# Optimization experiments

Measured on AMD Instinct MI355X. Metric: run time of the kernel, lower is better.

## Reference

```python
import jax, jax.numpy as jnp
import numpy as np
from jax import lax

B, H, W, C = 8, 128, 128, 256
HEADS, WIN, PRETRAIN = 8, 8, 8
QK_U = C // HEADS            # 32
QK_CH = QK_U * HEADS         # 256
KV_CH = QK_CH + C            # 512
BLOCK = WIN // 2             # key block size at half resolution
HALO = WIN                   # halo window (halo_window//2) at half resolution
PAD = (HALO - BLOCK) // 2    # halo overlap pad at half resolution


def _win_part(x, heads):
    b, h, w, c = x.shape
    u = c // heads
    x = x.reshape(b, h // WIN, WIN, w // WIN, WIN, heads, u)
    x = x.transpose(0, 1, 3, 5, 2, 4, 6)
    return x.reshape(b, (h // WIN) * (w // WIN), heads, WIN * WIN, u)


def _halo_part(x):
    # overlapping halo blocks: [b,hh,wh,c] -> [b, nw, HALO*HALO, c]
    b, h, w, c = x.shape
    xp = jnp.pad(x, ((0, 0), (PAD, PAD), (PAD, PAD), (0, 0)))
    hb, wb = h // BLOCK, w // BLOCK
    ih = jnp.arange(hb)[:, None] * BLOCK + jnp.arange(HALO)[None, :]
    iw = jnp.arange(wb)[:, None] * BLOCK + jnp.arange(HALO)[None, :]
    t = xp[:, ih][:, :, :, iw]            # [b, hb, HALO, wb, HALO, c]
    t = t.transpose(0, 1, 3, 2, 4, 5)
    return t.reshape(b, hb * wb, HALO * HALO, c)


def _halo_part_fused(x, heads):
    t = _halo_part(x)
    b, nw, l, c = t.shape
    u = c // heads
    return t.reshape(b, nw, l, heads, u).transpose(0, 1, 3, 2, 4)


def _l2n(x):
    # tf.math.l2_normalize with epsilon=1.55e-5
    return x * lax.rsqrt(jnp.maximum(jnp.sum(x * x, -1, keepdims=True), 1.55e-5))


def _rel_bias(cpb_w1, cpb_b1, cpb_w2):
    # Swin-V2 style continuous (log-CPB) relative bias between full-res query
    # window and half-res halo key window.
    qc = jnp.arange(WIN, dtype=jnp.float32)
    kc = (jnp.arange(HALO, dtype=jnp.float32) - PAD) * 2.0 + 0.5  # half-res centers in full-res coords
    r1 = qc[:, None] - kc[None, :]
    rel_y = jnp.broadcast_to(r1[:, None, :, None], (WIN, WIN, HALO, HALO))
    rel_x = jnp.broadcast_to(r1[None, :, None, :], (WIN, WIN, HALO, HALO))
    rel = jnp.stack([rel_y, rel_x], -1).reshape(WIN * WIN, HALO * HALO, 2)
    rel = rel / (PRETRAIN - 1) * 8.0
    rel = jnp.sign(rel) * jnp.log2(jnp.abs(rel) + 1.0) / np.float32(np.log2(8.0))
    hmid = jax.nn.relu(rel @ cpb_w1 + cpb_b1)
    bias = 16.0 * jax.nn.sigmoid(hmid @ cpb_w2)   # [q, k, heads]
    return bias.transpose(2, 0, 1)[None, None]    # [1,1,heads,q,k]


def _pad_mask(dtype):
    # No outer divisible-pad here (H,W divisible), but halo zero-padding at the
    # image border must be masked out (-100 on out-of-image key positions).
    m = jnp.ones((1, H // 2, W // 2, 1), dtype)   # min-pooled validity map (all ones)
    hm = _halo_part(m)                            # [1, nw, HALO*HALO, 1]; border halos -> 0
    return -100.0 * (hm[..., 0] == 0).astype(dtype)[:, :, None, None, :]  # [1,nw,1,1,k]


def reference(inputs, qkv_w, q_bias, v_bias, dw_w, dw_gamma, dw_beta, dw_mean, dw_var, scale, cpb_w1, cpb_b1, cpb_w2, proj_w, proj_b):
    qkv = jnp.einsum('bhwc,cd->bhwd', inputs, qkv_w)
    q, kv = qkv[..., :QK_CH], qkv[..., QK_CH:]
    # depthwise 3x3 stride-2 conv + (inference) batch-norm on K/V path
    kv = lax.conv_general_dilated(kv, dw_w, (2, 2), 'SAME',
                                  dimension_numbers=('NHWC', 'HWIO', 'NHWC'),
                                  feature_group_count=KV_CH)
    kv = (kv - dw_mean) * lax.rsqrt(dw_var + 1e-3) * dw_gamma + dw_beta
    q = q + q_bias
    kv = kv + jnp.concatenate([jnp.zeros_like(q_bias), v_bias])
    qw = _win_part(q, HEADS)                                 # [B,nw,h,64,QK_U]
    k = _halo_part_fused(kv[..., :QK_CH], HEADS)             # [B,nw,h,64,QK_U]
    v = _halo_part_fused(kv[..., QK_CH:], HEADS)             # [B,nw,h,64,V_U]
    logit_scale = jnp.exp(jnp.minimum(scale, np.float32(np.log(100.0))))  # [h,1,1]
    attn = jnp.einsum('bnhqd,bnhkd->bnhqk', _l2n(qw) * logit_scale, _l2n(k))
    attn = attn + _rel_bias(cpb_w1, cpb_b1, cpb_w2) + _pad_mask(attn.dtype)
    attn = jax.nn.softmax(attn, axis=-1)
    out = jnp.einsum('bnhqk,bnhkd->bnhqd', attn, v)
    hb, wb = H // WIN, W // WIN
    out = out.reshape(B, hb, wb, HEADS, WIN, WIN, C // HEADS)
    out = out.transpose(0, 1, 4, 2, 5, 3, 6).reshape(B, H, W, C)
    return jnp.einsum('bhwc,cd->bhwd', out, proj_w) + proj_b


def setup_inputs() -> dict:
    key = jax.random.key(0)
    ks = jax.random.split(key, 16)
    rn = lambda k, s, sc=0.05: jax.random.normal(k, s, jnp.float32) * sc
    return {
        'inputs': jax.random.normal(ks[0], (B, H, W, C), jnp.float32),
        'qkv_w': rn(ks[1], (C, 2 * QK_CH + C)),
        'q_bias': rn(ks[2], (QK_CH,)),
        'v_bias': rn(ks[3], (C,)),
        'dw_w': rn(ks[4], (3, 3, 1, KV_CH)),
        'dw_gamma': 1.0 + rn(ks[5], (KV_CH,)),
        'dw_beta': rn(ks[6], (KV_CH,)),
        'dw_mean': rn(ks[7], (KV_CH,)),
        'dw_var': jax.random.uniform(ks[8], (KV_CH,), jnp.float32, 0.5, 1.5),
        'scale': jnp.full((HEADS, 1, 1), np.log(10.0), jnp.float32),
        'cpb_w1': rn(ks[9], (2, 512), 0.5),
        'cpb_b1': rn(ks[10], (512,), 0.1),
        'cpb_w2': rn(ks[11], (512, HEADS), 0.1),
        'proj_w': rn(ks[12], (C, C)),
        'proj_b': rn(ks[13], (C,)),
    }
```

## Files before the change

kernel.cpp:

```cpp
#include <hip/hip_runtime.h>
#include <stdint.h>


typedef __attribute__((ext_vector_type(8))) short short8;
typedef __attribute__((ext_vector_type(4))) short short4v;
typedef __attribute__((ext_vector_type(4))) float f32x4;

#define VT_PLANE 4624L

__device__ __forceinline__ float bf2f(unsigned short u){
  union { unsigned int i; float f; } x; x.i = ((unsigned int)u)<<16; return x.f;
}
__device__ __forceinline__ unsigned short f2bf(float f){
  union { float f; unsigned int i; } x; x.f = f;
  unsigned int r = x.i + 0x7FFFu + ((x.i>>16)&1u);
  return (unsigned short)(r>>16);
}
__device__ __forceinline__ unsigned int pack_bf_t(float a, float b){
  union { float f; unsigned int u; } x, y; x.f = a; y.f = b;
  return (y.u & 0xFFFF0000u) | (x.u >> 16);
}
__device__ __forceinline__ void gl_lds16(const void* g, void* l){
  __builtin_amdgcn_global_load_lds((const __attribute__((address_space(1))) unsigned int*)g,
                                   (__attribute__((address_space(3))) unsigned int*)l, 16, 0, 0);
}

__global__ __launch_bounds__(256) void cvt_bf16_kernel(const float* __restrict__ in,
                                                       short* __restrict__ out, long n8)
{
  long stride = (long)gridDim.x * 256;
  for (long i = (long)blockIdx.x*256 + threadIdx.x; i < n8; i += stride){
    float4 a = ((const float4*)in)[2*i];
    float4 b = ((const float4*)in)[2*i+1];
    short8 v;
    v[0]=(short)f2bf(a.x); v[1]=(short)f2bf(a.y); v[2]=(short)f2bf(a.z); v[3]=(short)f2bf(a.w);
    v[4]=(short)f2bf(b.x); v[5]=(short)f2bf(b.y); v[6]=(short)f2bf(b.z); v[7]=(short)f2bf(b.w);
    ((short8*)out)[i] = v;
  }
}

__global__ void transpose_w_kernel(const float* __restrict__ w, short* __restrict__ wt,
                                   int K, int N)
{
  int idx = blockIdx.x*256 + threadIdx.x;
  if (idx >= K*N) return;
  int n = idx / K, k = idx - n*K;
  wt[idx] = (short)f2bf(w[(long)k*N + n]);
}

__global__ __launch_bounds__(64) void relbias_kernel(const float* __restrict__ w1,
    const float* __restrict__ b1, const float* __restrict__ w2, float* __restrict__ out)
{
  int q = blockIdx.x;
  int k = threadIdx.x;
  float ry = (float)(q>>3) - (((float)(k>>3) - 2.f)*2.f + 0.5f);
  float rx = (float)(q&7)  - (((float)(k&7)  - 2.f)*2.f + 0.5f);
  ry *= (8.f/7.f); rx *= (8.f/7.f);
  float sy = (ry>0.f)?1.f:((ry<0.f)?-1.f:0.f);
  float sx = (rx>0.f)?1.f:((rx<0.f)?-1.f:0.f);
  ry = sy * log2f(fabsf(ry)+1.f) * (1.f/3.f);
  rx = sx * log2f(fabsf(rx)+1.f) * (1.f/3.f);
  float acc[8] = {0,0,0,0,0,0,0,0};
  for (int j=0;j<512;j++){
    float hm = ry*w1[j] + rx*w1[512+j] + b1[j];
    hm = fmaxf(hm, 0.f);
#pragma unroll
    for (int h=0;h<8;h++) acc[h] += hm * w2[j*8+h];
  }
#pragma unroll
  for (int h=0;h<8;h++)
    out[h*4096 + q*64 + k] = (16.f / (1.f + __expf(-acc[h]))) * 1.4426950408889634f;
}

template<int ND, int OUTMODE>
__global__ __launch_bounds__(256) void gemm_bt_kernel(const short* __restrict__ A,
    const short* __restrict__ Bt, const float* __restrict__ bias,
    short* __restrict__ out_q, short* __restrict__ out_kv, float* __restrict__ out_f)
{
  __shared__ short smem[32768];
  const int tid  = threadIdx.x;
  const int lane = tid & 63;
  const int wid  = tid >> 6;
  const int wr = wid >> 1, wc = wid & 1;

  constexpr int NCB = ND / 128;
  const int bid = blockIdx.x;
  const int xcd = bid & 7;
  const int idx = bid >> 3;
  const long row0 = (long)(xcd * 128 + idx / NCB) * 128;
  const int  col0 = (idx % NCB) * 128;

  f32x4 acc[4][4];
#pragma unroll
  for (int m=0;m<4;m++)
#pragma unroll
    for (int n=0;n<4;n++) acc[m][n] = (f32x4){0.f,0.f,0.f,0.f};

  auto stage = [&](int buf, int kt){
#pragma unroll
    for (int j = 0; j < 4; j++) {
      int f = j*256 + tid;
      int r = f >> 3, p = f & 7;
      gl_lds16(A + (row0 + r)*256 + kt + ((p ^ (r&7))<<3),
               smem + buf*8192 + ((j*256 + (wid<<6))<<3));
      gl_lds16(Bt + (long)(col0 + r)*256 + kt + ((p ^ (r&7))<<3),
               smem + 16384 + buf*8192 + ((j*256 + (wid<<6))<<3));
    }
  };
  auto compute = [&](int buf){
    const short* As = smem + buf*8192;
    const short* Bs = smem + 16384 + buf*8192;
#pragma unroll
    for (int ks = 0; ks < 2; ks++) {
      short8 af[4], bfv[4];
#pragma unroll
      for (int m=0;m<4;m++){
        int r = wr*64 + m*16 + (lane & 15);
        int g = ks*4 + (lane >> 4);
        af[m] = *(const short8*)(As + r*64 + ((g ^ (r&7))<<3));
      }
#pragma unroll
      for (int n=0;n<4;n++){
        int r = wc*64 + n*16 + (lane & 15);
        int g = ks*4 + (lane >> 4);
        bfv[n] = *(const short8*)(Bs + r*64 + ((g ^ (r&7))<<3));
      }
#pragma unroll
      for (int m=0;m<4;m++)
#pragma unroll
        for (int n=0;n<4;n++)
          acc[m][n] = __builtin_amdgcn_mfma_f32_16x16x32_bf16(af[m], bfv[n], acc[m][n], 0, 0, 0);
    }
  };

  stage(0, 0);
  __syncthreads();
#pragma unroll
  for (int t = 0; t < 4; t++){
    if (t < 3) stage((t+1)&1, (t+1)*64);
    compute(t&1);
    __syncthreads();
  }

  if (OUTMODE == 0) {
    float bcol[4];
#pragma unroll
    for (int n=0;n<4;n++){
      int col = col0 + wc*64 + n*16 + (lane&15);
      bcol[n] = (col < 256) ? bias[col] : 0.f;
    }
#pragma unroll
    for (int m=0;m<4;m++){
#pragma unroll
      for (int n=0;n<4;n++){
        int col = wc*64 + n*16 + (lane&15);
        int cg = col >> 3;
#pragma unroll
        for (int rg=0;rg<4;rg++){
          int row = wr*64 + m*16 + ((lane>>4)<<2) + rg;
          smem[row*128 + ((cg ^ (row&7))<<3) + (col&7)] = (short)f2bf(acc[m][n][rg] + bcol[n]);
        }
      }
    }
    __syncthreads();
    int row = tid >> 1, ch = tid & 1;
    long grow = row0 + row;
#pragma unroll
    for (int j=0;j<8;j++){
      int cg = ch*8 + j;
      short8 v = *(const short8*)(smem + row*128 + ((cg ^ (row&7))<<3));
      int col = col0 + cg*8;
      if (col0 < 256) *(short8*)(out_q + grow*256 + col)        = v;
      else            *(short8*)(out_kv + grow*512 + (col-256)) = v;
    }
  } else {
    float* fs = (float*)smem;
#pragma unroll
    for (int m=0;m<4;m++){
#pragma unroll
      for (int n=0;n<4;n++){
        int col = wc*64 + n*16 + (lane&15);
        int c4 = col >> 2;
        float bv = bias[col0 + col];
#pragma unroll
        for (int rg=0;rg<4;rg++){
          int row = wr*64 + m*16 + ((lane>>4)<<2) + rg;
          fs[row*128 + ((c4 ^ (row&7))<<2) + (col&3)] = acc[m][n][rg] + bv;
        }
      }
    }
    __syncthreads();
    int row = tid >> 1;
    long grow = row0 + row;
#pragma unroll
    for (int j=0;j<16;j++){
      int c4 = (tid&1)*16 + j;
      float4 v = *(const float4*)(fs + row*128 + ((c4 ^ (row&7))<<2));
      *(float4*)(out_f + grow*ND + col0 + c4*4) = v;
    }
  }
}

__global__ __launch_bounds__(256) void dwconv_kernel(const short* __restrict__ kv_buf,
    const float* __restrict__ dw_w, const float* __restrict__ gamma,
    const float* __restrict__ beta, const float* __restrict__ mean,
    const float* __restrict__ var, const float* __restrict__ v_bias,
    short* __restrict__ kv_K, short* __restrict__ v_t)
{
  const int bid = blockIdx.x;
  const int b  = bid >> 7;
  const int rem = bid & 127;
  const int y2 = rem >> 1, xq = rem & 1;
  const int tid = threadIdx.x;
  const int lane = tid & 63, w = tid >> 6;
  const int ch0 = lane * 8;

  float s[8], sh[8];
#pragma unroll
  for (int i=0;i<8;i+=4){
    float4 g4 = *(const float4*)(gamma + ch0 + i);
    float4 v4 = *(const float4*)(var   + ch0 + i);
    float4 m4 = *(const float4*)(mean  + ch0 + i);
    float4 b4 = *(const float4*)(beta  + ch0 + i);
    float gg[4] = {g4.x,g4.y,g4.z,g4.w}, vv[4] = {v4.x,v4.y,v4.z,v4.w};
    float mm[4] = {m4.x,m4.y,m4.z,m4.w}, bb[4] = {b4.x,b4.y,b4.z,b4.w};
#pragma unroll
    for (int j=0;j<4;j++){
      float sv = gg[j] * rsqrtf(vv[j] + 1e-3f);
      s[i+j]  = sv;
      sh[i+j] = bb[j] - mm[j]*sv;
    }
  }
  if (ch0 >= 256){
    float4 vb0 = *(const float4*)(v_bias + ch0 - 256);
    float4 vb1 = *(const float4*)(v_bias + ch0 - 252);
    sh[0]+=vb0.x; sh[1]+=vb0.y; sh[2]+=vb0.z; sh[3]+=vb0.w;
    sh[4]+=vb1.x; sh[5]+=vb1.y; sh[6]+=vb1.z; sh[7]+=vb1.w;
  }

  float wv[9][8];
#pragma unroll
  for (int t=0;t<9;t++){
    float4 w0 = *(const float4*)(dw_w + t*512 + ch0);
    float4 w1 = *(const float4*)(dw_w + t*512 + ch0 + 4);
    wv[t][0]=w0.x; wv[t][1]=w0.y; wv[t][2]=w0.z; wv[t][3]=w0.w;
    wv[t][4]=w1.x; wv[t][5]=w1.y; wv[t][6]=w1.z; wv[t][7]=w1.w;
  }

  const int y0 = y2*2;
  const bool vy2 = (y0 + 2) < 128;
  const short* r0 = kv_buf + (((long)b*128 + y0)*128)*512 + ch0;
  const short* r1 = r0 + 128*512;
  const short* r2 = r1 + 128*512;
  const short8 zero8 = {0,0,0,0,0,0,0,0};

  const int x2base = xq*32 + w*8;
  const int xs = x2base*2;

  auto ld = [&](const short* r, int x, bool vy)->short8 {
    if (vy && x < 128) return *(const short8*)(r + (long)x*512);
    return zero8;
  };

  short8 L0 = ld(r0, xs, true), L1 = ld(r1, xs, true), L2 = ld(r2, xs, vy2);

  const int vc = ch0 - 256, hh = vc >> 5, d0 = vc & 31;
  const long vtb = ((long)((b*8+hh)*32 + d0))*VT_PLANE + (long)(y2+2)*68;

#pragma unroll
  for (int i=0;i<8;i++){
    const int x2 = x2base + i;
    const int xm = xs + 2*i + 1, xr = xs + 2*i + 2;
    short8 M0 = ld(r0, xm, true), M1 = ld(r1, xm, true), M2 = ld(r2, xm, vy2);
    short8 R0 = ld(r0, xr, true), R1 = ld(r1, xr, true), R2 = ld(r2, xr, vy2);

    float acc[8];
#pragma unroll
    for (int c=0;c<8;c++) acc[c] = 0.f;
#pragma unroll
    for (int c=0;c<8;c++){
      acc[c] += bf2f((unsigned short)L0[c]) * wv[0][c];
      acc[c] += bf2f((unsigned short)M0[c]) * wv[1][c];
      acc[c] += bf2f((unsigned short)R0[c]) * wv[2][c];
      acc[c] += bf2f((unsigned short)L1[c]) * wv[3][c];
      acc[c] += bf2f((unsigned short)M1[c]) * wv[4][c];
      acc[c] += bf2f((unsigned short)R1[c]) * wv[5][c];
      acc[c] += bf2f((unsigned short)L2[c]) * wv[6][c];
      acc[c] += bf2f((unsigned short)M2[c]) * wv[7][c];
      acc[c] += bf2f((unsigned short)R2[c]) * wv[8][c];
    }
    short8 o;
#pragma unroll
    for (int c=0;c<8;c++) o[c] = (short)f2bf(acc[c]*s[c] + sh[c]);

    if (ch0 < 256) {
      *(short8*)(kv_K + ((long)((b*64+y2)*64 + x2))*256 + ch0) = o;
    } else {
      long base = vtb + (x2+2);
#pragma unroll
      for (int c=0;c<8;c++) v_t[base + (long)c*VT_PLANE] = o[c];
    }
    L0 = R0; L1 = R1; L2 = R2;
  }
}

__global__ __launch_bounds__(256) void halo_attn_kernel(const short* __restrict__ q_buf,
    const short* __restrict__ kv_K, const short* __restrict__ v_t,
    const float* __restrict__ relb, const float* __restrict__ scale,
    short* __restrict__ attn_out)
{
  __shared__ short ps[4][4096];

  const int bid = blockIdx.x;
  const int b = bid >> 8, wno = bid & 255;
  const int bi = wno >> 4, bj = wno & 15;
  const int tid = threadIdx.x;
  const int w = tid >> 6, lane = tid & 63;
  const int g = lane >> 4, q15 = lane & 15;
  short* myps = &ps[w][0];
  const short8 zero8 = {0,0,0,0,0,0,0,0};

  long kbase[4]; bool kval[4];
#pragma unroll
  for (int m=0;m<4;m++){
    int key = m*16 + q15;
    int yy = bi*4-2 + (key>>3), xx = bj*4-2 + (key&7);
    kval[m] = (yy>=0 && yy<64 && xx>=0 && xx<64);
    kbase[m] = ((long)((b*64+yy)*64+xx))*256 + g*8;
  }
  float mkv[4][4];
#pragma unroll
  for (int m=0;m<4;m++)
#pragma unroll
    for (int r=0;r<4;r++){
      int key = m*16 + g*4 + r;
      int yy = bi*4-2+(key>>3), xx = bj*4-2+(key&7);
      mkv[m][r] = (yy>=0&&yy<64&&xx>=0&&xx<64) ? 0.f : -30000.f;
    }
  long qpix[4];
#pragma unroll
  for (int n=0;n<4;n++){
    int q = n*16+q15;
    qpix[n] = ((long)((b*128+bi*8+(q>>3))*128 + bj*8+(q&7)))*256;
  }
  int voff[2];
#pragma unroll
  for (int ks=0;ks<2;ks++) voff[ks] = (bi*4+ks*4+g)*68 + bj*4;

  for (int hi=0; hi<2; hi++){
    const int h = w + hi*4;
    const float lsc = __expf(fminf(scale[h], 4.6051702f)) * 1.4426950408889634f;

    short8 va[2][2];
#pragma unroll
    for (int dblk=0;dblk<2;dblk++){
      long pl = ((long)((b*8+h)*32 + dblk*16 + q15))*VT_PLANE;
#pragma unroll
      for (int ks=0;ks<2;ks++)
        va[dblk][ks] = *(const short8*)(v_t + pl + voff[ks]);
    }

    short8 af[4]; float rkk[4];
#pragma unroll
    for (int m=0;m<4;m++){
      af[m] = kval[m] ? *(const short8*)(kv_K + kbase[m] + h*32) : zero8;
      float ss = 0.f;
#pragma unroll
      for (int e=0;e<8;e++){ float f = bf2f((unsigned short)af[m][e]); ss += f*f; }
      ss += __shfl_xor(ss, 16);
      ss += __shfl_xor(ss, 32);
      rkk[m] = rsqrtf(fmaxf(ss, 1.55e-5f));
    }
    short8 bfv[4]; float rq[4];
#pragma unroll
    for (int n=0;n<4;n++){
      bfv[n] = *(const short8*)(q_buf + qpix[n] + h*32 + g*8);
      float ss = 0.f;
#pragma unroll
      for (int e=0;e<8;e++){ float f = bf2f((unsigned short)bfv[n][e]); ss += f*f; }
      ss += __shfl_xor(ss, 16);
      ss += __shfl_xor(ss, 32);
      rq[n] = rsqrtf(fmaxf(ss, 1.55e-5f)) * lsc;
    }
    float rk[4][4];
#pragma unroll
    for (int m=0;m<4;m++)
#pragma unroll
      for (int r=0;r<4;r++)
        rk[m][r] = __shfl(rkk[m], ((lane>>4)<<2) + r);

    f32x4 sc[4][4];
#pragma unroll
    for (int m=0;m<4;m++)
#pragma unroll
      for (int n=0;n<4;n++)
        sc[m][n] = __builtin_amdgcn_mfma_f32_16x16x32_bf16(af[m], bfv[n],
                       (f32x4){0.f,0.f,0.f,0.f}, 0, 0, 0);

    float mx[4] = {-3e38f,-3e38f,-3e38f,-3e38f};
#pragma unroll
    for (int m=0;m<4;m++){
#pragma unroll
      for (int n=0;n<4;n++){
        f32x4 rb = *(const f32x4*)(relb + h*4096 + (n*16+q15)*64 + m*16 + g*4);
#pragma unroll
        for (int r=0;r<4;r++){
          float v = sc[m][n][r] * (rk[m][r]*rq[n]) + rb[r] + mkv[m][r];
          sc[m][n][r] = v;
          mx[n] = fmaxf(mx[n], v);
        }
      }
    }
#pragma unroll
    for (int n=0;n<4;n++){
      mx[n] = fmaxf(mx[n], __shfl_xor(mx[n], 16));
      mx[n] = fmaxf(mx[n], __shfl_xor(mx[n], 32));
    }
    float sm[4] = {0.f,0.f,0.f,0.f};
#pragma unroll
    for (int m=0;m<4;m++)
#pragma unroll
      for (int n=0;n<4;n++)
#pragma unroll
        for (int r=0;r<4;r++){
          float e = exp2f(sc[m][n][r] - mx[n]);
          sc[m][n][r] = e;
          sm[n] += e;
        }
    float sminv[4];
#pragma unroll
    for (int n=0;n<4;n++){
      sm[n] += __shfl_xor(sm[n], 16);
      sm[n] += __shfl_xor(sm[n], 32);
      sminv[n] = 1.f / sm[n];
    }

#pragma unroll
    for (int n=0;n<4;n++){
      int row = n*16 + q15;
#pragma unroll
      for (int m=0;m<4;m++){
        uint2 pk;
        pk.x = pack_bf_t(sc[m][n][0], sc[m][n][1]);
        pk.y = pack_bf_t(sc[m][n][2], sc[m][n][3]);
        int kc = (m*2 + (g>>1)) ^ (row & 7);
        *(uint2*)(myps + row*64 + kc*8 + ((g&1)<<2)) = pk;
      }
    }
    asm volatile("s_waitcnt lgkmcnt(0)" ::: "memory");

    f32x4 oc[2][4];
#pragma unroll
    for (int dblk=0;dblk<2;dblk++)
#pragma unroll
      for (int n=0;n<4;n++) oc[dblk][n] = (f32x4){0.f,0.f,0.f,0.f};
#pragma unroll
    for (int ks=0;ks<2;ks++){
#pragma unroll
      for (int n=0;n<4;n++){
        int row = n*16 + q15;
        short8 pb = *(const short8*)(myps + row*64 + (((ks*4+g) ^ (row&7))<<3));
#pragma unroll
        for (int dblk=0;dblk<2;dblk++)
          oc[dblk][n] = __builtin_amdgcn_mfma_f32_16x16x32_bf16(va[dblk][ks], pb, oc[dblk][n], 0, 0, 0);
      }
    }

#pragma unroll
    for (int dblk=0;dblk<2;dblk++){
#pragma unroll
      for (int n=0;n<4;n++){
        uint2 pk;
        pk.x = pack_bf_t(oc[dblk][n][0]*sminv[n], oc[dblk][n][1]*sminv[n]);
        pk.y = pack_bf_t(oc[dblk][n][2]*sminv[n], oc[dblk][n][3]*sminv[n]);
        *(uint2*)(attn_out + qpix[n] + h*32 + dblk*16 + g*4) = pk;
      }
    }
  }
}

extern "C" void kernel_launch(void* const* d_in, const int* in_sizes, int n_in,
                              void* d_out, int out_size, void* d_ws, size_t ws_size,
                              hipStream_t stream)
{
  (void)in_sizes; (void)n_in; (void)out_size; (void)ws_size;
  const float* inputs = (const float*)d_in[0];
  const float* qkv_w  = (const float*)d_in[1];
  const float* q_bias = (const float*)d_in[2];
  const float* v_bias = (const float*)d_in[3];
  const float* dw_w   = (const float*)d_in[4];
  const float* dw_g   = (const float*)d_in[5];
  const float* dw_b   = (const float*)d_in[6];
  const float* dw_m   = (const float*)d_in[7];
  const float* dw_v   = (const float*)d_in[8];
  const float* scale  = (const float*)d_in[9];
  const float* cpb_w1 = (const float*)d_in[10];
  const float* cpb_b1 = (const float*)d_in[11];
  const float* cpb_w2 = (const float*)d_in[12];
  const float* proj_w = (const float*)d_in[13];
  const float* proj_b = (const float*)d_in[14];

  char* ws = (char*)d_ws;
  short* q_buf    = (short*)(ws);
  short* kv_buf   = (short*)(ws + 67108864L);
  short* kv_K     = (short*)(ws + 201326592L);
  short* v_t      = (short*)(ws + 218103808L);
  short* attn_buf = (short*)(ws + 237043712L);
  short* qkvw_t   = (short*)(ws + 304152576L);
  short* projw_t  = (short*)(ws + 304939008L);
  float* relb     = (float*)(ws + 305070080L);

  short* a_bf = attn_buf;

  cvt_bf16_kernel<<<2048, 256, 0, stream>>>(inputs, a_bf, 4194304L);
  transpose_w_kernel<<<768, 256, 0, stream>>>(qkv_w, qkvw_t, 256, 768);
  transpose_w_kernel<<<256, 256, 0, stream>>>(proj_w, projw_t, 256, 256);
  relbias_kernel<<<64, 64, 0, stream>>>(cpb_w1, cpb_b1, cpb_w2, relb);

  gemm_bt_kernel<768, 0><<<6144, 256, 0, stream>>>(
      a_bf, qkvw_t, q_bias, q_buf, kv_buf, nullptr);

  dwconv_kernel<<<1024, 256, 0, stream>>>(kv_buf, dw_w, dw_g, dw_b, dw_m, dw_v, v_bias,
                                          kv_K, v_t);

  halo_attn_kernel<<<2048, 256, 0, stream>>>(q_buf, kv_K, v_t, relb, scale, attn_buf);

  gemm_bt_kernel<256, 1><<<2048, 256, 0, stream>>>(
      attn_buf, projw_t, proj_b, nullptr, nullptr, (float*)d_out);
}
```

Baseline: 467.3 us.

## Process multiple M tiles per GEMM block and coalesce dwconv V-transpose stores via LDS

```diff
diff --git a/kernel.cpp b/kernel.cpp
--- a/kernel.cpp
+++ b/kernel.cpp
@@ -72,7 +72,7 @@
     out[h*4096 + q*64 + k] = (16.f / (1.f + __expf(-acc[h]))) * 1.4426950408889634f;
 }
 
-template<int ND, int OUTMODE>
+template<int ND, int OUTMODE, int MTILES>
 __global__ __launch_bounds__(256) void gemm_bt_kernel(const short* __restrict__ A,
     const short* __restrict__ Bt, const float* __restrict__ bias,
     short* __restrict__ out_q, short* __restrict__ out_kv, float* __restrict__ out_f)
@@ -82,12 +82,15 @@
   const int lane = tid & 63;
   const int wid  = tid >> 6;
   const int wr = wid >> 1, wc = wid & 1;
+  const int g = lane >> 4, q15 = lane & 15;
 
   constexpr int NCB = ND / 128;
+  constexpr int NSUP_X = (1024 / MTILES) / 8;
   const int bid = blockIdx.x;
   const int xcd = bid & 7;
   const int idx = bid >> 3;
-  const long row0 = (long)(xcd * 128 + idx / NCB) * 128;
+  const int sup = xcd * NSUP_X + idx / NCB;
+  const long row0 = (long)sup * (128 * MTILES);
   const int  col0 = (idx % NCB) * 128;
 
   f32x4 acc[4][4];
@@ -96,34 +99,37 @@
 #pragma unroll
     for (int n=0;n<4;n++) acc[m][n] = (f32x4){0.f,0.f,0.f,0.f};
 
-  auto stage = [&](int buf, int kt){
+  auto stage = [&](int s){
+    int buf = s & 1;
+    long rowt = row0 + (long)(s >> 2) * 128;
+    int kt = (s & 3) * 64;
 #pragma unroll
     for (int j = 0; j < 4; j++) {
       int f = j*256 + tid;
       int r = f >> 3, p = f & 7;
-      gl_lds16(A + (row0 + r)*256 + kt + ((p ^ (r&7))<<3),
-               smem + buf*8192 + ((j*256 + (wid<<6))<<3));
+      gl_lds16(A + (rowt + r)*256 + kt + ((p ^ (r&7))<<3),
+               smem + buf*16384 + ((j*256 + (wid<<6))<<3));
       gl_lds16(Bt + (long)(col0 + r)*256 + kt + ((p ^ (r&7))<<3),
-               smem + 16384 + buf*8192 + ((j*256 + (wid<<6))<<3));
+               smem + buf*16384 + 8192 + ((j*256 + (wid<<6))<<3));
     }
   };
   auto compute = [&](int buf){
-    const short* As = smem + buf*8192;
-    const short* Bs = smem + 16384 + buf*8192;
+    const short* As = smem + buf*16384;
+    const short* Bs = As + 8192;
 #pragma unroll
     for (int ks = 0; ks < 2; ks++) {
       short8 af[4], bfv[4];
 #pragma unroll
       for (int m=0;m<4;m++){
-        int r = wr*64 + m*16 + (lane & 15);
-        int g = ks*4 + (lane >> 4);
-        af[m] = *(const short8*)(As + r*64 + ((g ^ (r&7))<<3));
+        int r = wr*64 + m*16 + q15;
+        int gg = ks*4 + g;
+        af[m] = *(const short8*)(As + r*64 + ((gg ^ (r&7))<<3));
       }
 #pragma unroll
       for (int n=0;n<4;n++){
-        int r = wc*64 + n*16 + (lane & 15);
-        int g = ks*4 + (lane >> 4);
-        bfv[n] = *(const short8*)(Bs + r*64 + ((g ^ (r&7))<<3));
+        int r = wc*64 + n*16 + q15;
+        int gg = ks*4 + g;
+        bfv[n] = *(const short8*)(Bs + r*64 + ((gg ^ (r&7))<<3));
       }
 #pragma unroll
       for (int m=0;m<4;m++)
@@ -133,71 +139,86 @@
     }
   };
 
-  stage(0, 0);
+  stage(0);
   __syncthreads();
-#pragma unroll
-  for (int t = 0; t < 4; t++){
-    if (t < 3) stage((t+1)&1, (t+1)*64);
-    compute(t&1);
-    __syncthreads();
-  }
-
-  if (OUTMODE == 0) {
-    float bcol[4];
-#pragma unroll
-    for (int n=0;n<4;n++){
-      int col = col0 + wc*64 + n*16 + (lane&15);
-      bcol[n] = (col < 256) ? bias[col] : 0.f;
-    }
-#pragma unroll
-    for (int m=0;m<4;m++){
-#pragma unroll
-      for (int n=0;n<4;n++){
-        int col = wc*64 + n*16 + (lane&15);
-        int cg = col >> 3;
-#pragma unroll
-        for (int rg=0;rg<4;rg++){
-          int row = wr*64 + m*16 + ((lane>>4)<<2) + rg;
-          smem[row*128 + ((cg ^ (row&7))<<3) + (col&7)] = (short)f2bf(acc[m][n][rg] + bcol[n]);
+
+  for (int t = 0; t < MTILES; t++){
+#pragma unroll
+    for (int k = 0; k < 4; k++){
+      int s = t*4 + k;
+      if (s + 1 < MTILES*4) stage(s+1);
+      compute(s & 1);
+      __syncthreads();
+    }
+
+    if (OUTMODE == 0) {
+      short* sc = smem + 16384;
+#pragma unroll
+      for (int m=0;m<4;m++){
+#pragma unroll
+        for (int n=0;n<4;n++){
+          int col = wc*64 + n*16 + q15;
+          int cg = col >> 3;
+          float bv = (col0 + col < 256) ? bias[col0 + col] : 0.f;
+#pragma unroll
+          for (int rg=0;rg<4;rg++){
+            int row = wr*64 + m*16 + g*4 + rg;
+            sc[row*128 + ((cg ^ (row&7))<<3) + (col&7)] = (short)f2bf(acc[m][n][rg] + bv);
+          }
         }
       }
-    }
-    __syncthreads();
-    int row = tid >> 1, ch = tid & 1;
-    long grow = row0 + row;
-#pragma unroll
-    for (int j=0;j<8;j++){
-      int cg = ch*8 + j;
-      short8 v = *(const short8*)(smem + row*128 + ((cg ^ (row&7))<<3));
-      int col = col0 + cg*8;
-      if (col0 < 256) *(short8*)(out_q + grow*256 + col)        = v;
-      else            *(short8*)(out_kv + grow*512 + (col-256)) = v;
-    }
-  } else {
-    float* fs = (float*)smem;
-#pragma unroll
-    for (int m=0;m<4;m++){
-#pragma unroll
-      for (int n=0;n<4;n++){
-        int col = wc*64 + n*16 + (lane&15);
-        int c4 = col >> 2;
-        float bv = bias[col0 + col];
-#pragma unroll
-        for (int rg=0;rg<4;rg++){
-          int row = wr*64 + m*16 + ((lane>>4)<<2) + rg;
-          fs[row*128 + ((c4 ^ (row&7))<<2) + (col&3)] = acc[m][n][rg] + bv;
+      __syncthreads();
+      {
+        int row = tid >> 1, ch = tid & 1;
+        long grow = row0 + (long)t*128 + row;
+#pragma unroll
+        for (int j=0;j<8;j++){
+          int cg = ch*8 + j;
+          short8 v = *(const short8*)(sc + row*128 + ((cg ^ (row&7))<<3));
+          int col = col0 + cg*8;
+          if (col0 < 256) *(short8*)(out_q + grow*256 + col)        = v;
+          else            *(short8*)(out_kv + grow*512 + (col-256)) = v;
         }
       }
-    }
-    __syncthreads();
-    int row = tid >> 1;
-    long grow = row0 + row;
-#pragma unroll
-    for (int j=0;j<16;j++){
-      int c4 = (tid&1)*16 + j;
-      float4 v = *(const float4*)(fs + row*128 + ((c4 ^ (row&7))<<2));
-      *(float4*)(out_f + grow*ND + col0 + c4*4) = v;
-    }
+      __syncthreads();
+    } else {
+      float* fsc = (float*)(smem + 16384);
+#pragma unroll
+      for (int p=0;p<2;p++){
+        if (wr == p){
+#pragma unroll
+          for (int m=0;m<4;m++){
+#pragma unroll
+            for (int n=0;n<4;n++){
+              int col = wc*64 + n*16 + q15;
+              int c4 = col >> 2;
+              float bv = bias[col0 + col];
+#pragma unroll
+              for (int rg=0;rg<4;rg++){
+                int rl = m*16 + g*4 + rg;
+                fsc[rl*128 + ((c4 ^ (rl&7))<<2) + (col&3)] = acc[m][n][rg] + bv;
+              }
+            }
+          }
+        }
+        __syncthreads();
+        {
+          int rl = tid >> 2;
+          long grow = row0 + (long)t*128 + p*64 + rl;
+#pragma unroll
+          for (int j=0;j<8;j++){
+            int c4 = (tid&3)*8 + j;
+            float4 v = *(const float4*)(fsc + rl*128 + ((c4 ^ (rl&7))<<2));
+            *(float4*)(out_f + grow*ND + col0 + c4*4) = v;
+          }
+        }
+        __syncthreads();
+      }
+    }
+#pragma unroll
+    for (int m=0;m<4;m++)
+#pragma unroll
+      for (int n=0;n<4;n++) acc[m][n] = (f32x4){0.f,0.f,0.f,0.f};
   }
 }
 
@@ -207,6 +228,8 @@
     const float* __restrict__ var, const float* __restrict__ v_bias,
     short* __restrict__ kv_K, short* __restrict__ v_t)
 {
+  __shared__ short vls[32][256];
+
   const int bid = blockIdx.x;
   const int b  = bid >> 7;
   const int rem = bid & 127;
@@ -263,9 +286,6 @@
   };
 
   short8 L0 = ld(r0, xs, true), L1 = ld(r1, xs, true), L2 = ld(r2, xs, vy2);
-
-  const int vc = ch0 - 256, hh = vc >> 5, d0 = vc & 31;
-  const long vtb = ((long)((b*8+hh)*32 + d0))*VT_PLANE + (long)(y2+2)*68;
 
 #pragma unroll
   for (int i=0;i<8;i++){
@@ -296,11 +316,22 @@
     if (ch0 < 256) {
       *(short8*)(kv_K + ((long)((b*64+y2)*64 + x2))*256 + ch0) = o;
     } else {
-      long base = vtb + (x2+2);
-#pragma unroll
-      for (int c=0;c<8;c++) v_t[base + (long)c*VT_PLANE] = o[c];
+      *(short8*)(&vls[w*8 + i][ch0 - 256]) = o;
     }
     L0 = R0; L1 = R1; L2 = R2;
+  }
+
+  __syncthreads();
+  {
+    const int cc = tid, hh = cc >> 5, d0 = cc & 31;
+    long base = ((long)((b*8+hh)*32 + d0))*VT_PLANE + (long)(y2+2)*68 + xq*32 + 2;
+#pragma unroll
+    for (int j=0;j<16;j++){
+      short2 pr;
+      pr.x = vls[2*j][cc];
+      pr.y = vls[2*j+1][cc];
+      *(short2*)(v_t + base + 2*j) = pr;
+    }
   }
 }
 
@@ -517,7 +548,7 @@
   transpose_w_kernel<<<256, 256, 0, stream>>>(proj_w, projw_t, 256, 256);
   relbias_kernel<<<64, 64, 0, stream>>>(cpb_w1, cpb_b1, cpb_w2, relb);
 
-  gemm_bt_kernel<768, 0><<<6144, 256, 0, stream>>>(
+  gemm_bt_kernel<768, 0, 4><<<1536, 256, 0, stream>>>(
       a_bf, qkvw_t, q_bias, q_buf, kv_buf, nullptr);
 
   dwconv_kernel<<<1024, 256, 0, stream>>>(kv_buf, dw_w, dw_g, dw_b, dw_m, dw_v, v_bias,
@@ -525,6 +556,6 @@
 
   halo_attn_kernel<<<2048, 256, 0, stream>>>(q_buf, kv_K, v_t, relb, scale, attn_buf);
 
-  gemm_bt_kernel<256, 1><<<2048, 256, 0, stream>>>(
+  gemm_bt_kernel<256, 1, 4><<<512, 256, 0, stream>>>(
       attn_buf, projw_t, proj_b, nullptr, nullptr, (float*)d_out);
 }
```

New measurement: 426.7 us. 8.7% less time.
